# Kernel optimization log

Measured on AMD Instinct MI355X. Metric: run time of the kernel, lower is better.

Reference implementation:

```python
import jax, jax.numpy as jnp
import numpy as np

E = 64   # embed_dim
H = 64   # hidden_dim
U = 16384  # num users
T = 50   # max sequence length
NI = 100000  # num_items


def setup_inputs() -> dict:
    key = jax.random.key(0)
    k1, k2, k3, k4, k5, k6, k7 = jax.random.split(key, 7)
    sequences = jax.random.randint(k1, (U, T), 0, NI, dtype=jnp.int64 if jax.config.jax_enable_x64 else jnp.int32)
    lengths = jax.random.randint(k2, (U,), 1, T + 1, dtype=sequences.dtype)
    graph_embeddings = jax.random.normal(k3, (NI, E), dtype=jnp.float32)
    s = 1.0 / np.sqrt(H)
    W_ih = jax.random.uniform(k4, (4 * H, E), minval=-s, maxval=s, dtype=jnp.float32)
    W_hh = jax.random.uniform(k5, (4 * H, H), minval=-s, maxval=s, dtype=jnp.float32)
    b_ih = jax.random.uniform(k6, (4 * H,), minval=-s, maxval=s, dtype=jnp.float32)
    b_hh = jax.random.uniform(k7, (4 * H,), minval=-s, maxval=s, dtype=jnp.float32)
    return {"sequences": sequences, "lengths": lengths, "graph_embeddings": graph_embeddings,
            "W_ih": W_ih, "W_hh": W_hh, "b_ih": b_ih, "b_hh": b_hh, "num_items": NI}


def _lstm(x, W_ih, W_hh, b_ih, b_hh):
    # x: [B, T, E] -> outputs [B, T, H]; PyTorch gate order i, f, g, o
    B = x.shape[0]
    bias = b_ih + b_hh

    def step(carry, x_t):
        h, c = carry
        gates = x_t @ W_ih.T + h @ W_hh.T + bias  # [B, 4H]
        i, f, g, o = jnp.split(gates, 4, axis=-1)
        i = jax.nn.sigmoid(i)
        f = jax.nn.sigmoid(f)
        g = jnp.tanh(g)
        o = jax.nn.sigmoid(o)
        c = f * c + i * g
        h = o * jnp.tanh(c)
        return (h, c), h

    h0 = jnp.zeros((B, H), dtype=x.dtype)
    c0 = jnp.zeros((B, H), dtype=x.dtype)
    _, hs = jax.lax.scan(step, (h0, c0), jnp.swapaxes(x, 0, 1))  # [T, B, H]
    return jnp.swapaxes(hs, 0, 1)


def reference(sequences, lengths, graph_embeddings, W_ih, W_hh, b_ih, b_hh, num_items):
    x = graph_embeddings[sequences]            # [U, T, E] gather
    outs = _lstm(x, W_ih, W_hh, b_ih, b_hh)    # [U, T, H]
    valid = (jnp.arange(T)[None, :] < lengths[:, None]).astype(outs.dtype)  # [U, T]
    flat_ids = sequences.reshape(-1)
    flat_h = (outs * valid[:, :, None]).reshape(-1, H)
    sums = jax.ops.segment_sum(flat_h, flat_ids, num_segments=num_items)    # [NI, H]
    counts = jax.ops.segment_sum(valid.reshape(-1), flat_ids, num_segments=num_items)  # [NI]
    return jnp.where(counts[:, None] > 0, sums / jnp.maximum(counts[:, None], 1.0), 0.0)
```

## Files before the change

kernel.cpp:

```cpp
#include <hip/hip_runtime.h>

#define EDIM 64
#define HDIM 64

typedef short bf16x8 __attribute__((ext_vector_type(8)));
typedef float f32x4  __attribute__((ext_vector_type(4)));

__device__ __forceinline__ float fast_sigmoid(float x) {
    return __builtin_amdgcn_rcpf(1.0f + __builtin_amdgcn_exp2f(-1.4426950408889634f * x));
}
__device__ __forceinline__ float fast_tanh(float x) {
    return 1.0f - 2.0f * __builtin_amdgcn_rcpf(1.0f + __builtin_amdgcn_exp2f(2.8853900817779268f * x));
}
__device__ __forceinline__ unsigned short f2bf(float f) {
    unsigned int u = __float_as_uint(f);
    return (unsigned short)((u + 0x7FFF + ((u >> 16) & 1)) >> 16);
}
__device__ __forceinline__ bf16x8 pack8(float4 a, float4 b) {
    bf16x8 w;
    w[0]=(short)f2bf(a.x); w[1]=(short)f2bf(a.y); w[2]=(short)f2bf(a.z); w[3]=(short)f2bf(a.w);
    w[4]=(short)f2bf(b.x); w[5]=(short)f2bf(b.y); w[6]=(short)f2bf(b.z); w[7]=(short)f2bf(b.w);
    return w;
}
__device__ __forceinline__ int hu_of(int hb, int q, int r) {
    return ((hb >> 1) << 5) + (q << 3) + ((hb & 1) << 2) + r;
}

__global__ void k_hist(const int* __restrict__ lens, int U, int* __restrict__ hist) {
    int u = blockIdx.x * 256 + threadIdx.x;
    if (u < U) atomicAdd(&hist[lens[u]], 1);
}
__global__ void k_scan(const int* __restrict__ hist, int* __restrict__ off) {
    if (threadIdx.x == 0) { int s = 0; for (int l = 50; l >= 1; --l) { off[l] = s; s += hist[l]; } off[0] = s; }
}
__global__ void k_place(const int* __restrict__ lens, int U, int* __restrict__ off, int* __restrict__ order) {
    int u = blockIdx.x * 256 + threadIdx.x;
    if (u < U) { int p = atomicAdd(&off[lens[u]], 1); order[p] = u; }
}

__global__ __launch_bounds__(256, 1) void lstm_wave(
    const int* __restrict__ seq, const int* __restrict__ lens,
    const float* __restrict__ emb,
    const float* __restrict__ W_ih, const float* __restrict__ W_hh,
    const float* __restrict__ b_ih, const float* __restrict__ b_hh,
    const int* __restrict__ order,
    float* __restrict__ out_sum, float* __restrict__ cnt,
    int U, int T)
{
    __shared__ __align__(16) unsigned char lds[32768 + 4 * 4096];
    const int tid  = threadIdx.x;
    const int wv   = tid >> 6;
    const int lane = tid & 63;
    const int su   = lane & 15;
    const int q    = lane >> 4;

    for (int s = tid; s < 2048; s += 256) {
        const int rt = s >> 7, kt = (s >> 6) & 1, l = s & 63;
        const int g = rt >> 2, hb = rt & 3;
        const int rho = l & 15, qf = l >> 4;
        const int grow = g * 64 + hu_of(hb, rho >> 2, rho & 3);
        const float* src = W_ih + (size_t)grow * EDIM + kt * 32 + qf * 8;
        float4 a = *reinterpret_cast<const float4*>(src);
        float4 b = *reinterpret_cast<const float4*>(src + 4);
        *reinterpret_cast<bf16x8*>(lds + (size_t)s * 16) = pack8(a, b);
    }

    bf16x8 whreg[4][4][2];
    {
        const int rho = lane & 15, qf = lane >> 4;
        #pragma unroll
        for (int g = 0; g < 4; ++g)
            #pragma unroll
            for (int hb = 0; hb < 4; ++hb) {
                const int grow = g * 64 + hu_of(hb, rho >> 2, rho & 3);
                const float* src = W_hh + (size_t)grow * HDIM + qf * 8;
                #pragma unroll
                for (int kp = 0; kp < 2; ++kp) {
                    float4 a = *reinterpret_cast<const float4*>(src + kp * 32);
                    float4 b = *reinterpret_cast<const float4*>(src + kp * 32 + 4);
                    whreg[g][hb][kp] = pack8(a, b);
                }
            }
    }
    f32x4 biasv[4][4];
    #pragma unroll
    for (int g = 0; g < 4; ++g)
        #pragma unroll
        for (int hb = 0; hb < 4; ++hb)
            #pragma unroll
            for (int r = 0; r < 4; ++r) {
                const int grow = g * 64 + hu_of(hb, q, r);
                biasv[g][hb][r] = b_ih[grow] + b_hh[grow];
            }

    __syncthreads();

    const int nblk = gridDim.x;
    const int wbase = (wv * nblk + blockIdx.x) * 16;
    int us = 0, len = 0;
    if (wbase + su < U) { us = order[wbase + su]; len = lens[us]; }
    const int* sp = seq + (size_t)us * T;
    const int mT = __shfl(len, 0, 64);
    if (mT == 0) return;

    const float4* e4 = reinterpret_cast<const float4*>(emb);
    int itc = sp[0];
    int itn = (mT > 1) ? sp[1] : itc;
    bf16x8 bx0, bx1, bh0 = {0,0,0,0,0,0,0,0}, bh1 = {0,0,0,0,0,0,0,0};
    {
        const size_t eb = (size_t)itc * 16 + q * 2;
        float4 xa = e4[eb], xb = e4[eb + 1], xc = e4[eb + 8], xd = e4[eb + 9];
        bx0 = pack8(xa, xb); bx1 = pack8(xc, xd);
    }
    f32x4 cst[4] = {{0,0,0,0},{0,0,0,0},{0,0,0,0},{0,0,0,0}};
    const int XP = 32768 + wv * 4096;

    for (int t = 0; t < mT; ++t) {
        float4 na, nb, nc, nd; int sn = itn;
        const bool pf = (t + 1 < mT);
        if (pf) {
            const size_t eb = (size_t)itn * 16 + q * 2;
            na = e4[eb]; nb = e4[eb + 1]; nc = e4[eb + 8]; nd = e4[eb + 9];
        }
        if (t + 2 < mT) sn = sp[t + 2];

        f32x4 hn[4];
        #pragma unroll
        for (int hb = 0; hb < 4; ++hb) {
            bf16x8 wx0[4], wx1[4];
            #pragma unroll
            for (int g = 0; g < 4; ++g) {
                const int rt = g * 4 + hb;
                wx0[g] = *reinterpret_cast<const bf16x8*>(lds + ((rt * 2 + 0) * 64 + lane) * 16);
                wx1[g] = *reinterpret_cast<const bf16x8*>(lds + ((rt * 2 + 1) * 64 + lane) * 16);
            }
            f32x4 acc[4];
            #pragma unroll
            for (int g = 0; g < 4; ++g) {
                acc[g] = biasv[g][hb];
                acc[g] = __builtin_amdgcn_mfma_f32_16x16x32_bf16(wx0[g], bx0, acc[g], 0, 0, 0);
                acc[g] = __builtin_amdgcn_mfma_f32_16x16x32_bf16(wx1[g], bx1, acc[g], 0, 0, 0);
                acc[g] = __builtin_amdgcn_mfma_f32_16x16x32_bf16(whreg[g][hb][0], bh0, acc[g], 0, 0, 0);
                acc[g] = __builtin_amdgcn_mfma_f32_16x16x32_bf16(whreg[g][hb][1], bh1, acc[g], 0, 0, 0);
            }
            #pragma unroll
            for (int r = 0; r < 4; ++r) {
                const float gi = fast_sigmoid(acc[0][r]);
                const float gf = fast_sigmoid(acc[1][r]);
                const float gg = fast_tanh   (acc[2][r]);
                const float go = fast_sigmoid(acc[3][r]);
                const float cc = gf * cst[hb][r] + gi * gg;
                cst[hb][r] = cc;
                hn[hb][r] = go * fast_tanh(cc);
            }
        }
        bh0[0]=(short)f2bf(hn[0][0]); bh0[1]=(short)f2bf(hn[0][1]); bh0[2]=(short)f2bf(hn[0][2]); bh0[3]=(short)f2bf(hn[0][3]);
        bh0[4]=(short)f2bf(hn[1][0]); bh0[5]=(short)f2bf(hn[1][1]); bh0[6]=(short)f2bf(hn[1][2]); bh0[7]=(short)f2bf(hn[1][3]);
        bh1[0]=(short)f2bf(hn[2][0]); bh1[1]=(short)f2bf(hn[2][1]); bh1[2]=(short)f2bf(hn[2][2]); bh1[3]=(short)f2bf(hn[2][3]);
        bh1[4]=(short)f2bf(hn[3][0]); bh1[5]=(short)f2bf(hn[3][1]); bh1[6]=(short)f2bf(hn[3][2]); bh1[7]=(short)f2bf(hn[3][3]);

        const bool val = (t < len);
        #pragma unroll
        for (int hb = 0; hb < 4; ++hb) {
            f32x4 w4;
            #pragma unroll
            for (int r = 0; r < 4; ++r) w4[r] = val ? hn[hb][r] : 0.0f;
            int byte = (su * 64 + hu_of(hb, q, 0)) * 4;
            byte ^= (su & 7) << 4;
            *reinterpret_cast<f32x4*>(lds + XP + byte) = w4;
        }
        asm volatile("s_waitcnt lgkmcnt(0)" ::: "memory");
        #pragma unroll
        for (int g = 0; g < 16; ++g) {
            const int itg = __shfl(itc, g, 64);
            int byte = (g * 64 + lane) * 4;
            byte ^= (g & 7) << 4;
            const float hv = *reinterpret_cast<const float*>(lds + XP + byte);
            atomicAdd(&out_sum[(size_t)itg * HDIM + lane], hv);
        }
        if (q == 0 && val) atomicAdd(&cnt[itc], 1.0f);

        if (pf) { bx0 = pack8(na, nb); bx1 = pack8(nc, nd); itc = itn; itn = sn; }
    }
}

__global__ __launch_bounds__(256) void finalize_mean(
    float* __restrict__ out, const float* __restrict__ cnt, int NI)
{
    const int idx = blockIdx.x * blockDim.x + threadIdx.x;
    const int total = NI * (HDIM / 4);
    if (idx >= total) return;
    const int i = idx >> 4;
    const float c = cnt[i];
    const float s = (c > 0.0f) ? __builtin_amdgcn_rcpf(c) : 0.0f;
    float4* o = reinterpret_cast<float4*>(out);
    float4 v = o[idx];
    v.x *= s; v.y *= s; v.z *= s; v.w *= s;
    o[idx] = v;
}

extern "C" void kernel_launch(void* const* d_in, const int* in_sizes, int n_in,
                              void* d_out, int out_size, void* d_ws, size_t ws_size,
                              hipStream_t stream)
{
    const int*   seq  = (const int*)d_in[0];
    const int*   lens = (const int*)d_in[1];
    const float* emb  = (const float*)d_in[2];
    const float* W_ih = (const float*)d_in[3];
    const float* W_hh = (const float*)d_in[4];
    const float* b_ih = (const float*)d_in[5];
    const float* b_hh = (const float*)d_in[6];
    float* out = (float*)d_out;

    const int U  = in_sizes[1];
    const int T  = in_sizes[0] / U;
    const int NI = in_sizes[2] / EDIM;

    float* cnt   = (float*)d_ws;
    int*   hist  = (int*)d_ws + NI;
    int*   off   = hist + 64;
    int*   order = off + 64;

    hipMemsetAsync(out, 0, (size_t)NI * HDIM * sizeof(float), stream);
    hipMemsetAsync(d_ws, 0, ((size_t)NI + 128) * sizeof(float), stream);

    const int ublk = (U + 255) / 256;
    k_hist <<<ublk, 256, 0, stream>>>(lens, U, hist);
    k_scan <<<1, 64, 0, stream>>>(hist, off);
    k_place<<<ublk, 256, 0, stream>>>(lens, U, off, order);

    const int nblk = (U + 63) / 64;
    lstm_wave<<<nblk, 256, 0, stream>>>(seq, lens, emb, W_ih, W_hh, b_ih, b_hh,
                                        order, out, cnt, U, T);

    const int total = NI * (HDIM / 4);
    finalize_mean<<<(total + 255) / 256, 256, 0, stream>>>(out, cnt, NI);
}
```

Before: 306.5 us.

## Fold activation scales into weights, keep W_ih in registers, defer scatter, fuse sort

```diff
diff --git a/kernel.cpp b/kernel.cpp
--- a/kernel.cpp
+++ b/kernel.cpp
@@ -2,40 +2,45 @@
 
 #define EDIM 64
 #define HDIM 64
+#define S_SIG  (-1.4426950408889634f)
+#define S_TANH ( 2.8853900817779268f)
 
 typedef short bf16x8 __attribute__((ext_vector_type(8)));
 typedef float f32x4  __attribute__((ext_vector_type(4)));
 
-__device__ __forceinline__ float fast_sigmoid(float x) {
-    return __builtin_amdgcn_rcpf(1.0f + __builtin_amdgcn_exp2f(-1.4426950408889634f * x));
-}
-__device__ __forceinline__ float fast_tanh(float x) {
-    return 1.0f - 2.0f * __builtin_amdgcn_rcpf(1.0f + __builtin_amdgcn_exp2f(2.8853900817779268f * x));
-}
+__device__ __forceinline__ float rcp_(float x){ return __builtin_amdgcn_rcpf(x); }
+__device__ __forceinline__ float exp2_(float x){ return __builtin_amdgcn_exp2f(x); }
 __device__ __forceinline__ unsigned short f2bf(float f) {
     unsigned int u = __float_as_uint(f);
     return (unsigned short)((u + 0x7FFF + ((u >> 16) & 1)) >> 16);
 }
-__device__ __forceinline__ bf16x8 pack8(float4 a, float4 b) {
+__device__ __forceinline__ bf16x8 pack8s(float4 a, float4 b, float s) {
     bf16x8 w;
-    w[0]=(short)f2bf(a.x); w[1]=(short)f2bf(a.y); w[2]=(short)f2bf(a.z); w[3]=(short)f2bf(a.w);
-    w[4]=(short)f2bf(b.x); w[5]=(short)f2bf(b.y); w[6]=(short)f2bf(b.z); w[7]=(short)f2bf(b.w);
+    w[0]=(short)f2bf(a.x*s); w[1]=(short)f2bf(a.y*s); w[2]=(short)f2bf(a.z*s); w[3]=(short)f2bf(a.w*s);
+    w[4]=(short)f2bf(b.x*s); w[5]=(short)f2bf(b.y*s); w[6]=(short)f2bf(b.z*s); w[7]=(short)f2bf(b.w*s);
     return w;
+}
+__device__ __forceinline__ unsigned int cvtpk(float lo, float hi) {
+    unsigned int r;
+    asm("v_cvt_pk_bf16_f32 %0, %1, %2" : "=v"(r) : "v"(lo), "v"(hi));
+    return r;
 }
 __device__ __forceinline__ int hu_of(int hb, int q, int r) {
     return ((hb >> 1) << 5) + (q << 3) + ((hb & 1) << 2) + r;
 }
 
-__global__ void k_hist(const int* __restrict__ lens, int U, int* __restrict__ hist) {
-    int u = blockIdx.x * 256 + threadIdx.x;
-    if (u < U) atomicAdd(&hist[lens[u]], 1);
-}
-__global__ void k_scan(const int* __restrict__ hist, int* __restrict__ off) {
-    if (threadIdx.x == 0) { int s = 0; for (int l = 50; l >= 1; --l) { off[l] = s; s += hist[l]; } off[0] = s; }
-}
-__global__ void k_place(const int* __restrict__ lens, int U, int* __restrict__ off, int* __restrict__ order) {
-    int u = blockIdx.x * 256 + threadIdx.x;
-    if (u < U) { int p = atomicAdd(&off[lens[u]], 1); order[p] = u; }
+__global__ __launch_bounds__(1024) void k_sort(const int* __restrict__ lens, int U,
+                                               int* __restrict__ order) {
+    __shared__ int hist[52];
+    __shared__ int base[52];
+    const int tid = threadIdx.x;
+    if (tid < 52) hist[tid] = 0;
+    __syncthreads();
+    for (int u = tid; u < U; u += 1024) atomicAdd(&hist[lens[u]], 1);
+    __syncthreads();
+    if (tid == 0) { int s = 0; for (int l = 50; l >= 0; --l) { base[l] = s; s += hist[l]; } }
+    __syncthreads();
+    for (int u = tid; u < U; u += 1024) { int p = atomicAdd(&base[lens[u]], 1); order[p] = u; }
 }
 
 __global__ __launch_bounds__(256, 1) void lstm_wave(
@@ -47,73 +52,85 @@
     float* __restrict__ out_sum, float* __restrict__ cnt,
     int U, int T)
 {
-    __shared__ __align__(16) unsigned char lds[32768 + 4 * 4096];
+    __shared__ __align__(16) unsigned char lds[4 * 4096];
     const int tid  = threadIdx.x;
     const int wv   = tid >> 6;
     const int lane = tid & 63;
     const int su   = lane & 15;
     const int q    = lane >> 4;
 
-    for (int s = tid; s < 2048; s += 256) {
-        const int rt = s >> 7, kt = (s >> 6) & 1, l = s & 63;
-        const int g = rt >> 2, hb = rt & 3;
-        const int rho = l & 15, qf = l >> 4;
-        const int grow = g * 64 + hu_of(hb, rho >> 2, rho & 3);
-        const float* src = W_ih + (size_t)grow * EDIM + kt * 32 + qf * 8;
-        float4 a = *reinterpret_cast<const float4*>(src);
-        float4 b = *reinterpret_cast<const float4*>(src + 4);
-        *reinterpret_cast<bf16x8*>(lds + (size_t)s * 16) = pack8(a, b);
+    bf16x8 wx[4][4][2], wh[4][4][2];
+    f32x4  biasv[4][4];
+    #pragma unroll
+    for (int g = 0; g < 4; ++g) {
+        const float s = (g == 2) ? S_TANH : S_SIG;
+        #pragma unroll
+        for (int hb = 0; hb < 4; ++hb) {
+            const int grow = g * 64 + hu_of(hb, su >> 2, su & 3);
+            const float* wi = W_ih + (size_t)grow * EDIM + q * 8;
+            const float* wp = W_hh + (size_t)grow * HDIM + q * 8;
+            #pragma unroll
+            for (int kp = 0; kp < 2; ++kp) {
+                float4 a = *reinterpret_cast<const float4*>(wi + kp * 32);
+                float4 b = *reinterpret_cast<const float4*>(wi + kp * 32 + 4);
+                wx[g][hb][kp] = pack8s(a, b, s);
+                float4 c2 = *reinterpret_cast<const float4*>(wp + kp * 32);
+                float4 d2 = *reinterpret_cast<const float4*>(wp + kp * 32 + 4);
+                wh[g][hb][kp] = pack8s(c2, d2, s);
+            }
+            #pragma unroll
+            for (int r = 0; r < 4; ++r) {
+                const int gi2 = g * 64 + hu_of(hb, q, r);
+                biasv[g][hb][r] = s * (b_ih[gi2] + b_hh[gi2]);
+            }
+        }
     }
 
-    bf16x8 whreg[4][4][2];
-    {
-        const int rho = lane & 15, qf = lane >> 4;
-        #pragma unroll
-        for (int g = 0; g < 4; ++g)
-            #pragma unroll
-            for (int hb = 0; hb < 4; ++hb) {
-                const int grow = g * 64 + hu_of(hb, rho >> 2, rho & 3);
-                const float* src = W_hh + (size_t)grow * HDIM + qf * 8;
-                #pragma unroll
-                for (int kp = 0; kp < 2; ++kp) {
-                    float4 a = *reinterpret_cast<const float4*>(src + kp * 32);
-                    float4 b = *reinterpret_cast<const float4*>(src + kp * 32 + 4);
-                    whreg[g][hb][kp] = pack8(a, b);
-                }
-            }
-    }
-    f32x4 biasv[4][4];
-    #pragma unroll
-    for (int g = 0; g < 4; ++g)
-        #pragma unroll
-        for (int hb = 0; hb < 4; ++hb)
-            #pragma unroll
-            for (int r = 0; r < 4; ++r) {
-                const int grow = g * 64 + hu_of(hb, q, r);
-                biasv[g][hb][r] = b_ih[grow] + b_hh[grow];
-            }
-
-    __syncthreads();
-
     const int nblk = gridDim.x;
-    const int wbase = (wv * nblk + blockIdx.x) * 16;
+    const int grp  = (wv & 1) ? ((wv + 1) * nblk - 1 - blockIdx.x)
+                              : (wv * nblk + blockIdx.x);
+    const int wbase = grp * 16;
     int us = 0, len = 0;
     if (wbase + su < U) { us = order[wbase + su]; len = lens[us]; }
     const int* sp = seq + (size_t)us * T;
-    const int mT = __shfl(len, 0, 64);
-    if (mT == 0) return;
+    int mT = len;
+    mT = max(mT, __shfl_xor(mT, 1, 64));
+    mT = max(mT, __shfl_xor(mT, 2, 64));
+    mT = max(mT, __shfl_xor(mT, 4, 64));
+    mT = max(mT, __shfl_xor(mT, 8, 64));
+    if (mT <= 0) return;
 
     const float4* e4 = reinterpret_cast<const float4*>(emb);
     int itc = sp[0];
-    int itn = (mT > 1) ? sp[1] : itc;
+    int itn = (1 < mT) ? sp[1] : itc;
     bf16x8 bx0, bx1, bh0 = {0,0,0,0,0,0,0,0}, bh1 = {0,0,0,0,0,0,0,0};
     {
         const size_t eb = (size_t)itc * 16 + q * 2;
-        float4 xa = e4[eb], xb = e4[eb + 1], xc = e4[eb + 8], xd = e4[eb + 9];
-        bx0 = pack8(xa, xb); bx1 = pack8(xc, xd);
+        bx0 = pack8s(e4[eb],     e4[eb + 1], 1.0f);
+        bx1 = pack8s(e4[eb + 8], e4[eb + 9], 1.0f);
     }
     f32x4 cst[4] = {{0,0,0,0},{0,0,0,0},{0,0,0,0},{0,0,0,0}};
-    const int XP = 32768 + wv * 4096;
+    f32x4 hs[4];
+    int   itp = 0, vprev = 0;
+    const int XP = wv * 4096;
+
+    auto scatter_prev = [&]() {
+        #pragma unroll
+        for (int hb = 0; hb < 4; ++hb) {
+            int byte = (su * 64 + hu_of(hb, q, 0)) * 4;
+            byte ^= (su & 7) << 4;
+            *reinterpret_cast<f32x4*>(lds + XP + byte) = hs[hb];
+        }
+        asm volatile("s_waitcnt lgkmcnt(0)" ::: "memory");
+        #pragma unroll
+        for (int g = 0; g < 16; ++g) {
+            const int itg = __builtin_amdgcn_readlane(itp, g);
+            const int byte = ((g * 64 + lane) * 4) ^ ((g & 7) << 4);
+            const float hv = *reinterpret_cast<const float*>(lds + XP + byte);
+            atomicAdd(&out_sum[(size_t)itg * HDIM + lane], hv);
+        }
+        if (q == 0 && vprev) atomicAdd(&cnt[itp], 1.0f);
+    };
 
     for (int t = 0; t < mT; ++t) {
         float4 na, nb, nc, nd; int sn = itn;
@@ -124,64 +141,56 @@
         }
         if (t + 2 < mT) sn = sp[t + 2];
 
+        if (t > 0) scatter_prev();
+
         f32x4 hn[4];
         #pragma unroll
         for (int hb = 0; hb < 4; ++hb) {
-            bf16x8 wx0[4], wx1[4];
-            #pragma unroll
-            for (int g = 0; g < 4; ++g) {
-                const int rt = g * 4 + hb;
-                wx0[g] = *reinterpret_cast<const bf16x8*>(lds + ((rt * 2 + 0) * 64 + lane) * 16);
-                wx1[g] = *reinterpret_cast<const bf16x8*>(lds + ((rt * 2 + 1) * 64 + lane) * 16);
-            }
             f32x4 acc[4];
             #pragma unroll
             for (int g = 0; g < 4; ++g) {
                 acc[g] = biasv[g][hb];
-                acc[g] = __builtin_amdgcn_mfma_f32_16x16x32_bf16(wx0[g], bx0, acc[g], 0, 0, 0);
-                acc[g] = __builtin_amdgcn_mfma_f32_16x16x32_bf16(wx1[g], bx1, acc[g], 0, 0, 0);
-                acc[g] = __builtin_amdgcn_mfma_f32_16x16x32_bf16(whreg[g][hb][0], bh0, acc[g], 0, 0, 0);
-                acc[g] = __builtin_amdgcn_mfma_f32_16x16x32_bf16(whreg[g][hb][1], bh1, acc[g], 0, 0, 0);
+                acc[g] = __builtin_amdgcn_mfma_f32_16x16x32_bf16(wx[g][hb][0], bx0, acc[g], 0, 0, 0);
+                acc[g] = __builtin_amdgcn_mfma_f32_16x16x32_bf16(wx[g][hb][1], bx1, acc[g], 0, 0, 0);
+                acc[g] = __builtin_amdgcn_mfma_f32_16x16x32_bf16(wh[g][hb][0], bh0, acc[g], 0, 0, 0);
+                acc[g] = __builtin_amdgcn_mfma_f32_16x16x32_bf16(wh[g][hb][1], bh1, acc[g], 0, 0, 0);
             }
             #pragma unroll
             for (int r = 0; r < 4; ++r) {
-                const float gi = fast_sigmoid(acc[0][r]);
-                const float gf = fast_sigmoid(acc[1][r]);
-                const float gg = fast_tanh   (acc[2][r]);
-                const float go = fast_sigmoid(acc[3][r]);
+                const float ei = exp2_(acc[0][r]);
+                const float ef = exp2_(acc[1][r]);
+                const float eg = exp2_(acc[2][r]);
+                const float eo = exp2_(acc[3][r]);
+                const float gi = rcp_(1.0f + ei);
+                const float gf = rcp_(1.0f + ef);
+                const float gg = 1.0f - 2.0f * rcp_(1.0f + eg);
+                const float go = rcp_(1.0f + eo);
                 const float cc = gf * cst[hb][r] + gi * gg;
                 cst[hb][r] = cc;
-                hn[hb][r] = go * fast_tanh(cc);
-            }
-        }
-        bh0[0]=(short)f2bf(hn[0][0]); bh0[1]=(short)f2bf(hn[0][1]); bh0[2]=(short)f2bf(hn[0][2]); bh0[3]=(short)f2bf(hn[0][3]);
-        bh0[4]=(short)f2bf(hn[1][0]); bh0[5]=(short)f2bf(hn[1][1]); bh0[6]=(short)f2bf(hn[1][2]); bh0[7]=(short)f2bf(hn[1][3]);
-        bh1[0]=(short)f2bf(hn[2][0]); bh1[1]=(short)f2bf(hn[2][1]); bh1[2]=(short)f2bf(hn[2][2]); bh1[3]=(short)f2bf(hn[2][3]);
-        bh1[4]=(short)f2bf(hn[3][0]); bh1[5]=(short)f2bf(hn[3][1]); bh1[6]=(short)f2bf(hn[3][2]); bh1[7]=(short)f2bf(hn[3][3]);
-
-        const bool val = (t < len);
-        #pragma unroll
-        for (int hb = 0; hb < 4; ++hb) {
-            f32x4 w4;
-            #pragma unroll
-            for (int r = 0; r < 4; ++r) w4[r] = val ? hn[hb][r] : 0.0f;
-            int byte = (su * 64 + hu_of(hb, q, 0)) * 4;
-            byte ^= (su & 7) << 4;
-            *reinterpret_cast<f32x4*>(lds + XP + byte) = w4;
-        }
-        asm volatile("s_waitcnt lgkmcnt(0)" ::: "memory");
-        #pragma unroll
-        for (int g = 0; g < 16; ++g) {
-            const int itg = __shfl(itc, g, 64);
-            int byte = (g * 64 + lane) * 4;
-            byte ^= (g & 7) << 4;
-            const float hv = *reinterpret_cast<const float*>(lds + XP + byte);
-            atomicAdd(&out_sum[(size_t)itg * HDIM + lane], hv);
-        }
-        if (q == 0 && val) atomicAdd(&cnt[itc], 1.0f);
-
-        if (pf) { bx0 = pack8(na, nb); bx1 = pack8(nc, nd); itc = itn; itn = sn; }
+                const float et = exp2_(S_TANH * cc);
+                const float th = 1.0f - 2.0f * rcp_(1.0f + et);
+                hn[hb][r] = go * th;
+            }
+        }
+        uint4 p0, p1;
+        p0.x = cvtpk(hn[0][0], hn[0][1]); p0.y = cvtpk(hn[0][2], hn[0][3]);
+        p0.z = cvtpk(hn[1][0], hn[1][1]); p0.w = cvtpk(hn[1][2], hn[1][3]);
+        p1.x = cvtpk(hn[2][0], hn[2][1]); p1.y = cvtpk(hn[2][2], hn[2][3]);
+        p1.z = cvtpk(hn[3][0], hn[3][1]); p1.w = cvtpk(hn[3][2], hn[3][3]);
+        bh0 = __builtin_bit_cast(bf16x8, p0);
+        bh1 = __builtin_bit_cast(bf16x8, p1);
+
+        const int val = (t < len) ? 1 : 0;
+        const float vm = val ? 1.0f : 0.0f;
+        #pragma unroll
+        for (int hb = 0; hb < 4; ++hb)
+            #pragma unroll
+            for (int r = 0; r < 4; ++r) hs[hb][r] = hn[hb][r] * vm;
+        itp = itc; vprev = val;
+
+        if (pf) { bx0 = pack8s(na, nb, 1.0f); bx1 = pack8s(nc, nd, 1.0f); itc = itn; itn = sn; }
     }
+    scatter_prev();
 }
 
 __global__ __launch_bounds__(256) void finalize_mean(
@@ -217,17 +226,12 @@
     const int NI = in_sizes[2] / EDIM;
 
     float* cnt   = (float*)d_ws;
-    int*   hist  = (int*)d_ws + NI;
-    int*   off   = hist + 64;
-    int*   order = off + 64;
+    int*   order = (int*)d_ws + NI;
 
     hipMemsetAsync(out, 0, (size_t)NI * HDIM * sizeof(float), stream);
-    hipMemsetAsync(d_ws, 0, ((size_t)NI + 128) * sizeof(float), stream);
-
-    const int ublk = (U + 255) / 256;
-    k_hist <<<ublk, 256, 0, stream>>>(lens, U, hist);
-    k_scan <<<1, 64, 0, stream>>>(hist, off);
-    k_place<<<ublk, 256, 0, stream>>>(lens, U, off, order);
+    hipMemsetAsync(cnt, 0, (size_t)NI * sizeof(float), stream);
+
+    k_sort<<<1, 1024, 0, stream>>>(lens, U, order);
 
     const int nblk = (U + 63) / 64;
     lstm_wave<<<nblk, 256, 0, stream>>>(seq, lens, emb, W_ih, W_hh, b_ih, b_hh,
```

After: 299.4 us. 2.3% less time.
